# Performance work log

Measured on AMD Instinct MI355X. Metric: run time of the kernel, lower is better.

Reference implementation:

```python
import jax, jax.numpy as jnp
import numpy as np

N_NODES = 100000
N_EDGES = 1600000
DIM = 64
LAYERS = 2


def setup_inputs() -> dict:
    key = jax.random.key(0)
    k1, k2, k3, k4 = jax.random.split(key, 4)
    h = jax.random.normal(k1, (N_NODES, DIM), dtype=jnp.float32)
    w = jax.random.uniform(k2, (N_EDGES,), dtype=jnp.float32)
    src = jax.random.randint(k3, (N_EDGES,), 0, N_NODES, dtype=jnp.int32)
    dst = jax.random.randint(k4, (N_EDGES,), 0, N_NODES, dtype=jnp.int32)
    return {"h": h, "w": w, "src": src, "dst": dst}


def reference(h, w, src, dst):
    N = h.shape[0]
    # weighted in-degree, clamped at 1 (DGL in_degrees(weight='w').clamp(min=1))
    deg = jnp.maximum(jax.ops.segment_sum(w, dst, num_segments=N), 1.0)
    norm = deg[:, None] ** -0.5  # [N, 1]
    embs = [h]
    for _ in range(LAYERS):
        h_norm = h * norm                              # [N, d]
        m = h_norm[src] * w[:, None]                   # [E, d] edge messages (u_mul_e)
        neigh_sum = jax.ops.segment_sum(m, dst, num_segments=N)  # fn.sum
        h = neigh_sum * norm
        embs.append(h)
    # mean over [h0, h1, ..., hL]
    return jnp.mean(jnp.stack(embs, axis=1), axis=1)
```

## Files before the change

kernel.cpp:

```cpp
#include <hip/hip_runtime.h>
#include <hip/hip_bf16.h>

#define D 64
#define THREADS 256
#define BKT_BITS 9
#define BKT_NODES (1 << BKT_BITS)
#define CHUNK 8192

__device__ __forceinline__ unsigned f2bf(float f) {
    unsigned u = __float_as_uint(f);
    return (u + 0x7fffu + ((u >> 16) & 1u)) >> 16;
}
__device__ __forceinline__ float2 bfpair(unsigned v) {
    return make_float2(__uint_as_float(v << 16), __uint_as_float(v & 0xffff0000u));
}

__global__ void p1a_hist(const int* __restrict__ dst, int* __restrict__ blockCount,
                         int E, int B) {
    __shared__ int lc[256];
    int t = threadIdx.x;
    lc[t] = 0;
    __syncthreads();
    int base = blockIdx.x * CHUNK;
    int end = min(base + CHUNK, E);
    for (int e = base + t; e < end; e += THREADS)
        atomicAdd(&lc[dst[e] >> BKT_BITS], 1);
    __syncthreads();
    if (t < B) blockCount[(long long)blockIdx.x * B + t] = lc[t];
}

__global__ void p1b_scanblocks(int* __restrict__ blockCount, int* __restrict__ total,
                               int NBLK, int B) {
    __shared__ int sm[256];
    int b = blockIdx.x, t = threadIdx.x;
    int run = 0;
    for (int base = 0; base < NBLK; base += 256) {
        int i = base + t;
        int v = (i < NBLK) ? blockCount[(long long)i * B + b] : 0;
        sm[t] = v;
        __syncthreads();
        for (int off = 1; off < 256; off <<= 1) {
            int u = (t >= off) ? sm[t - off] : 0;
            __syncthreads();
            sm[t] += u;
            __syncthreads();
        }
        if (i < NBLK) blockCount[(long long)i * B + b] = run + sm[t] - v;
        run += sm[255];
        __syncthreads();
    }
    if (t == 0) total[b] = run;
}

__global__ void p1c_scanbuckets(const int* __restrict__ total, int* __restrict__ bstart,
                                int B, int E) {
    __shared__ int sm[256];
    int t = threadIdx.x;
    int run = 0;
    for (int base = 0; base < B; base += 256) {
        int i = base + t;
        int v = (i < B) ? total[i] : 0;
        sm[t] = v;
        __syncthreads();
        for (int off = 1; off < 256; off <<= 1) {
            int u = (t >= off) ? sm[t - off] : 0;
            __syncthreads();
            sm[t] += u;
            __syncthreads();
        }
        if (i < B) bstart[i] = run + sm[t] - v;
        run += sm[255];
        __syncthreads();
    }
    if (t == 0) bstart[B] = E;
}

__global__ void p1d_scatter(const int* __restrict__ dst, const int* __restrict__ src,
                            const float* __restrict__ w, const int* __restrict__ blockCount,
                            const int* __restrict__ bstart, int2* __restrict__ temp,
                            int E, int B) {
    __shared__ int cur[256];
    int t = threadIdx.x;
    if (t < B) cur[t] = bstart[t] + blockCount[(long long)blockIdx.x * B + t];
    __syncthreads();
    int base = blockIdx.x * CHUNK;
    int end = min(base + CHUNK, E);
    for (int e = base + t; e < end; e += THREADS) {
        int d = dst[e];
        int b = d >> BKT_BITS;
        int pos = atomicAdd(&cur[b], 1);
        temp[pos] = make_int2(src[e] | ((d & (BKT_NODES - 1)) << 17),
                              __float_as_int(w[e]));
    }
}

__global__ void p2_build(const int2* __restrict__ temp, const int* __restrict__ bstart,
                         int2* __restrict__ packed, int* __restrict__ rowptr,
                         float* __restrict__ norm, int N, int E, int B) {
    __shared__ int cnt[BKT_NODES];
    __shared__ float degs[BKT_NODES];
    __shared__ int cur[BKT_NODES];
    __shared__ int sm[256];
    int b = blockIdx.x, t = threadIdx.x;
    int ebeg = bstart[b], eend = bstart[b + 1];
    for (int i = t; i < BKT_NODES; i += THREADS) { cnt[i] = 0; degs[i] = 0.0f; }
    __syncthreads();
    for (int e = ebeg + t; e < eend; e += THREADS) {
        int2 pk = temp[e];
        int dl = (pk.x >> 17) & (BKT_NODES - 1);
        atomicAdd(&cnt[dl], 1);
        atomicAdd(&degs[dl], __int_as_float(pk.y));
    }
    __syncthreads();
    int run = 0;
    for (int base = 0; base < BKT_NODES; base += 256) {
        int v = cnt[base + t];
        sm[t] = v;
        __syncthreads();
        for (int off = 1; off < 256; off <<= 1) {
            int u = (t >= off) ? sm[t - off] : 0;
            __syncthreads();
            sm[t] += u;
            __syncthreads();
        }
        cur[base + t] = run + sm[t] - v;
        run += sm[255];
        __syncthreads();
    }
    int node0 = b << BKT_BITS;
    for (int i = t; i < BKT_NODES; i += THREADS) {
        int node = node0 + i;
        if (node < N) {
            rowptr[node] = ebeg + cur[i];
            norm[node] = rsqrtf(fmaxf(degs[i], 1.0f));
        }
    }
    if (b == 0 && t == 0) rowptr[N] = E;
    __syncthreads();
    for (int e = ebeg + t; e < eend; e += THREADS) {
        int2 pk = temp[e];
        int dl = (pk.x >> 17) & (BKT_NODES - 1);
        int pos = atomicAdd(&cur[dl], 1);
        packed[ebeg + pos] = make_int2(pk.x & 0x1ffff, pk.y);
    }
}

__global__ void tobf16_kernel(const float* __restrict__ h, unsigned* __restrict__ hbf2,
                              long long nd4) {
    long long i = (long long)blockIdx.x * blockDim.x + threadIdx.x;
    if (i < nd4) {
        float4 v = ((const float4*)h)[i];
        ((uint2*)hbf2)[i] = make_uint2(f2bf(v.x) | (f2bf(v.y) << 16),
                                       f2bf(v.z) | (f2bf(v.w) << 16));
    }
}

__global__ void gather1_kernel(const uint2* __restrict__ h_in, const int2* __restrict__ packed,
                               const int* __restrict__ rowptr, const float* __restrict__ norm,
                               uint2* __restrict__ h_out, int N) {
    int node = blockIdx.x * (blockDim.x >> 4) + (threadIdx.x >> 4);
    int lane = threadIdx.x & 15;
    if (node >= N) return;
    int j = rowptr[node], end = rowptr[node + 1];
    float a00 = 0, a01 = 0, a02 = 0, a03 = 0;
    float a10 = 0, a11 = 0, a12 = 0, a13 = 0;
    float a20 = 0, a21 = 0, a22 = 0, a23 = 0;
    float a30 = 0, a31 = 0, a32 = 0, a33 = 0;
    for (; j + 4 <= end; j += 4) {
        int2 p0 = packed[j], p1 = packed[j + 1], p2 = packed[j + 2], p3 = packed[j + 3];
        uint2 r0 = h_in[((long long)p0.x << 4) + lane];
        uint2 r1 = h_in[((long long)p1.x << 4) + lane];
        uint2 r2 = h_in[((long long)p2.x << 4) + lane];
        uint2 r3 = h_in[((long long)p3.x << 4) + lane];
        float c0 = __int_as_float(p0.y) * norm[p0.x];
        float c1 = __int_as_float(p1.y) * norm[p1.x];
        float c2 = __int_as_float(p2.y) * norm[p2.x];
        float c3 = __int_as_float(p3.y) * norm[p3.x];
        float2 f0a = bfpair(r0.x), f0b = bfpair(r0.y);
        float2 f1a = bfpair(r1.x), f1b = bfpair(r1.y);
        float2 f2a = bfpair(r2.x), f2b = bfpair(r2.y);
        float2 f3a = bfpair(r3.x), f3b = bfpair(r3.y);
        a00 = fmaf(f0a.x, c0, a00); a01 = fmaf(f0a.y, c0, a01);
        a02 = fmaf(f0b.x, c0, a02); a03 = fmaf(f0b.y, c0, a03);
        a10 = fmaf(f1a.x, c1, a10); a11 = fmaf(f1a.y, c1, a11);
        a12 = fmaf(f1b.x, c1, a12); a13 = fmaf(f1b.y, c1, a13);
        a20 = fmaf(f2a.x, c2, a20); a21 = fmaf(f2a.y, c2, a21);
        a22 = fmaf(f2b.x, c2, a22); a23 = fmaf(f2b.y, c2, a23);
        a30 = fmaf(f3a.x, c3, a30); a31 = fmaf(f3a.y, c3, a31);
        a32 = fmaf(f3b.x, c3, a32); a33 = fmaf(f3b.y, c3, a33);
    }
    for (; j < end; ++j) {
        int2 p = packed[j];
        uint2 r = h_in[((long long)p.x << 4) + lane];
        float c = __int_as_float(p.y) * norm[p.x];
        float2 fa = bfpair(r.x), fb = bfpair(r.y);
        a00 = fmaf(fa.x, c, a00); a01 = fmaf(fa.y, c, a01);
        a02 = fmaf(fb.x, c, a02); a03 = fmaf(fb.y, c, a03);
    }
    float nv = norm[node];
    float d0 = ((a00 + a10) + (a20 + a30)) * nv;
    float d1 = ((a01 + a11) + (a21 + a31)) * nv;
    float d2 = ((a02 + a12) + (a22 + a32)) * nv;
    float d3 = ((a03 + a13) + (a23 + a33)) * nv;
    h_out[((long long)node << 4) + lane] =
        make_uint2(f2bf(d0) | (f2bf(d1) << 16), f2bf(d2) | (f2bf(d3) << 16));
}

__global__ void gather2_final_kernel(const uint2* __restrict__ h0bf, const uint2* __restrict__ h1bf,
                                     const int2* __restrict__ packed, const int* __restrict__ rowptr,
                                     const float* __restrict__ norm, float* __restrict__ out, int N) {
    int node = blockIdx.x * (blockDim.x >> 4) + (threadIdx.x >> 4);
    int lane = threadIdx.x & 15;
    if (node >= N) return;
    int j = rowptr[node], end = rowptr[node + 1];
    float a00 = 0, a01 = 0, a02 = 0, a03 = 0;
    float a10 = 0, a11 = 0, a12 = 0, a13 = 0;
    float a20 = 0, a21 = 0, a22 = 0, a23 = 0;
    float a30 = 0, a31 = 0, a32 = 0, a33 = 0;
    for (; j + 4 <= end; j += 4) {
        int2 p0 = packed[j], p1 = packed[j + 1], p2 = packed[j + 2], p3 = packed[j + 3];
        uint2 r0 = h1bf[((long long)p0.x << 4) + lane];
        uint2 r1 = h1bf[((long long)p1.x << 4) + lane];
        uint2 r2 = h1bf[((long long)p2.x << 4) + lane];
        uint2 r3 = h1bf[((long long)p3.x << 4) + lane];
        float c0 = __int_as_float(p0.y) * norm[p0.x];
        float c1 = __int_as_float(p1.y) * norm[p1.x];
        float c2 = __int_as_float(p2.y) * norm[p2.x];
        float c3 = __int_as_float(p3.y) * norm[p3.x];
        float2 f0a = bfpair(r0.x), f0b = bfpair(r0.y);
        float2 f1a = bfpair(r1.x), f1b = bfpair(r1.y);
        float2 f2a = bfpair(r2.x), f2b = bfpair(r2.y);
        float2 f3a = bfpair(r3.x), f3b = bfpair(r3.y);
        a00 = fmaf(f0a.x, c0, a00); a01 = fmaf(f0a.y, c0, a01);
        a02 = fmaf(f0b.x, c0, a02); a03 = fmaf(f0b.y, c0, a03);
        a10 = fmaf(f1a.x, c1, a10); a11 = fmaf(f1a.y, c1, a11);
        a12 = fmaf(f1b.x, c1, a12); a13 = fmaf(f1b.y, c1, a13);
        a20 = fmaf(f2a.x, c2, a20); a21 = fmaf(f2a.y, c2, a21);
        a22 = fmaf(f2b.x, c2, a22); a23 = fmaf(f2b.y, c2, a23);
        a30 = fmaf(f3a.x, c3, a30); a31 = fmaf(f3a.y, c3, a31);
        a32 = fmaf(f3b.x, c3, a32); a33 = fmaf(f3b.y, c3, a33);
    }
    for (; j < end; ++j) {
        int2 p = packed[j];
        uint2 r = h1bf[((long long)p.x << 4) + lane];
        float c = __int_as_float(p.y) * norm[p.x];
        float2 fa = bfpair(r.x), fb = bfpair(r.y);
        a00 = fmaf(fa.x, c, a00); a01 = fmaf(fa.y, c, a01);
        a02 = fmaf(fb.x, c, a02); a03 = fmaf(fb.y, c, a03);
    }
    long long idx = ((long long)node << 4) + lane;
    float nv = norm[node];
    uint2 h0r = h0bf[idx], h1r = h1bf[idx];
    float2 h0a = bfpair(h0r.x), h0b = bfpair(h0r.y);
    float2 h1a = bfpair(h1r.x), h1b = bfpair(h1r.y);
    float4 o;
    o.x = (h0a.x + h1a.x + ((a00 + a10) + (a20 + a30)) * nv) * (1.0f / 3.0f);
    o.y = (h0a.y + h1a.y + ((a01 + a11) + (a21 + a31)) * nv) * (1.0f / 3.0f);
    o.z = (h0b.x + h1b.x + ((a02 + a12) + (a22 + a32)) * nv) * (1.0f / 3.0f);
    o.w = (h0b.y + h1b.y + ((a03 + a13) + (a23 + a33)) * nv) * (1.0f / 3.0f);
    ((float4*)out)[idx] = o;
}

extern "C" void kernel_launch(void* const* d_in, const int* in_sizes, int n_in,
                              void* d_out, int out_size, void* d_ws, size_t ws_size,
                              hipStream_t stream) {
    const float* h   = (const float*)d_in[0];
    const float* w   = (const float*)d_in[1];
    const int*   src = (const int*)d_in[2];
    const int*   dst = (const int*)d_in[3];
    const int N = in_sizes[0] / D;
    const int E = in_sizes[1];
    float* out = (float*)d_out;

    const int B = (N + BKT_NODES - 1) >> BKT_BITS;
    const int NBLK = (E + CHUNK - 1) / CHUNK;

    char* ws = (char*)d_ws;
    size_t off = 0;
    auto alloc = [&](size_t bytes, size_t align) -> char* {
        off = (off + align - 1) & ~(align - 1);
        char* p = ws + off;
        off += bytes;
        return p;
    };
    float* norm     = (float*)alloc((size_t)N * 4, 16);
    int*   rowptr   = (int*)  alloc((size_t)(N + 1) * 4, 16);
    int*   total    = (int*)  alloc((size_t)B * 4, 16);
    int*   bstart   = (int*)  alloc((size_t)(B + 1) * 4, 16);
    int*   blockCnt = (int*)  alloc((size_t)NBLK * B * 4, 16);
    int2*  packed   = (int2*) alloc((size_t)E * 8, 16);
    char*  shared_region = alloc((size_t)E * 8, 128);
    int2*     temp = (int2*)shared_region;
    unsigned* h1bf = (unsigned*)shared_region;
    unsigned* h0bf = (unsigned*)alloc((size_t)N * D * 2, 128);

    const int nodes_per_block = THREADS / 16;
    const int gather_blocks = (N + nodes_per_block - 1) / nodes_per_block;
    const long long nd4 = (long long)N * D / 4;
    const int cvt_blocks = (int)((nd4 + THREADS - 1) / THREADS);

    p1a_hist<<<NBLK, THREADS, 0, stream>>>(dst, blockCnt, E, B);
    p1b_scanblocks<<<B, 256, 0, stream>>>(blockCnt, total, NBLK, B);
    p1c_scanbuckets<<<1, 256, 0, stream>>>(total, bstart, B, E);
    p1d_scatter<<<NBLK, THREADS, 0, stream>>>(dst, src, w, blockCnt, bstart, temp, E, B);
    p2_build<<<B, 256, 0, stream>>>(temp, bstart, packed, rowptr, norm, N, E, B);

    tobf16_kernel<<<cvt_blocks, THREADS, 0, stream>>>(h, h0bf, nd4);

    gather1_kernel<<<gather_blocks, THREADS, 0, stream>>>((const uint2*)h0bf, packed, rowptr,
                                                          norm, (uint2*)h1bf, N);
    gather2_final_kernel<<<gather_blocks, THREADS, 0, stream>>>((const uint2*)h0bf, (const uint2*)h1bf,
                                                                packed, rowptr, norm, out, N);
}
```

Before: 234.3 us.

## Pad CSR rows to multiples of four, prefold source norm, use 16B gathers

The CSR build is split into two kernels. The first computes degree norms and padded row starts, with each row rounded up to a multiple of four. The second places edges with the weight already multiplied by norm[src] and fills padding slots with zero-weight entries. The gather kernels then run a tail-free loop that reads edge pairs with int4 loads, drops the per-edge norm gather, and uses 8 lanes per node with 16-byte bf16 row loads instead of 16 lanes with 8-byte loads. The cost is an extra launch, extra padded edge traffic and more registers per thread.

```diff
diff --git a/kernel.cpp b/kernel.cpp
--- a/kernel.cpp
+++ b/kernel.cpp
@@ -6,6 +6,7 @@
 #define BKT_BITS 9
 #define BKT_NODES (1 << BKT_BITS)
 #define CHUNK 8192
+#define PADMAX 1540
 
 __device__ __forceinline__ unsigned f2bf(float f) {
     unsigned u = __float_as_uint(f);
@@ -94,13 +95,13 @@
     }
 }
 
-__global__ void p2_build(const int2* __restrict__ temp, const int* __restrict__ bstart,
-                         int2* __restrict__ packed, int* __restrict__ rowptr,
-                         float* __restrict__ norm, int N, int E, int B) {
+__global__ void p2a_norm(const int2* __restrict__ temp, const int* __restrict__ bstart,
+                         int* __restrict__ rowptrP, float* __restrict__ norm,
+                         int N, int E, int B) {
     __shared__ int cnt[BKT_NODES];
     __shared__ float degs[BKT_NODES];
-    __shared__ int cur[BKT_NODES];
     __shared__ int sm[256];
+    __shared__ int rowst[BKT_NODES];
     int b = blockIdx.x, t = threadIdx.x;
     int ebeg = bstart[b], eend = bstart[b + 1];
     for (int i = t; i < BKT_NODES; i += THREADS) { cnt[i] = 0; degs[i] = 0.0f; }
@@ -114,7 +115,7 @@
     __syncthreads();
     int run = 0;
     for (int base = 0; base < BKT_NODES; base += 256) {
-        int v = cnt[base + t];
+        int v = (cnt[base + t] + 3) & ~3;
         sm[t] = v;
         __syncthreads();
         for (int off = 1; off < 256; off <<= 1) {
@@ -123,25 +124,45 @@
             sm[t] += u;
             __syncthreads();
         }
-        cur[base + t] = run + sm[t] - v;
+        rowst[base + t] = run + sm[t] - v;
         run += sm[255];
         __syncthreads();
     }
+    int pbase = ((ebeg + 3) & ~3) + PADMAX * b;
     int node0 = b << BKT_BITS;
     for (int i = t; i < BKT_NODES; i += THREADS) {
+        rowptrP[node0 + i] = pbase + rowst[i];
         int node = node0 + i;
-        if (node < N) {
-            rowptr[node] = ebeg + cur[i];
-            norm[node] = rsqrtf(fmaxf(degs[i], 1.0f));
-        }
-    }
-    if (b == 0 && t == 0) rowptr[N] = E;
+        if (node < N) norm[node] = rsqrtf(fmaxf(degs[i], 1.0f));
+    }
+    if (b == B - 1 && t == 0)
+        rowptrP[(long long)B << BKT_BITS] = ((E + 3) & ~3) + PADMAX * B;
+}
+
+__global__ void p2b_place(const int2* __restrict__ temp, const int* __restrict__ bstart,
+                          const int* __restrict__ rowptrP, const float* __restrict__ norm,
+                          int2* __restrict__ packed, int N, int B) {
+    __shared__ int cur[BKT_NODES];
+    int b = blockIdx.x, t = threadIdx.x;
+    int ebeg = bstart[b], eend = bstart[b + 1];
+    int node0 = b << BKT_BITS;
+    for (int i = t; i < BKT_NODES; i += THREADS) cur[i] = rowptrP[node0 + i];
     __syncthreads();
     for (int e = ebeg + t; e < eend; e += THREADS) {
         int2 pk = temp[e];
         int dl = (pk.x >> 17) & (BKT_NODES - 1);
+        int s = pk.x & 0x1ffff;
         int pos = atomicAdd(&cur[dl], 1);
-        packed[ebeg + pos] = make_int2(pk.x & 0x1ffff, pk.y);
+        float c = __int_as_float(pk.y) * norm[s];
+        packed[pos] = make_int2(s, __float_as_int(c));
+    }
+    __syncthreads();
+    for (int i = t; i < BKT_NODES; i += THREADS) {
+        int node = node0 + i;
+        if (node >= N) continue;
+        int tail = cur[i];
+        int next = rowptrP[node0 + i + 1];
+        for (int p = tail; p < next; ++p) packed[p] = make_int2(0, 0);
     }
 }
 
@@ -155,110 +176,113 @@
     }
 }
 
-__global__ void gather1_kernel(const uint2* __restrict__ h_in, const int2* __restrict__ packed,
+__global__ void gather1_kernel(const uint4* __restrict__ h_in, const int2* __restrict__ packed,
                                const int* __restrict__ rowptr, const float* __restrict__ norm,
-                               uint2* __restrict__ h_out, int N) {
-    int node = blockIdx.x * (blockDim.x >> 4) + (threadIdx.x >> 4);
-    int lane = threadIdx.x & 15;
+                               uint4* __restrict__ h_out, int N) {
+    int node = blockIdx.x * (blockDim.x >> 3) + (threadIdx.x >> 3);
+    int lane = threadIdx.x & 7;
     if (node >= N) return;
     int j = rowptr[node], end = rowptr[node + 1];
-    float a00 = 0, a01 = 0, a02 = 0, a03 = 0;
-    float a10 = 0, a11 = 0, a12 = 0, a13 = 0;
-    float a20 = 0, a21 = 0, a22 = 0, a23 = 0;
-    float a30 = 0, a31 = 0, a32 = 0, a33 = 0;
-    for (; j + 4 <= end; j += 4) {
-        int2 p0 = packed[j], p1 = packed[j + 1], p2 = packed[j + 2], p3 = packed[j + 3];
-        uint2 r0 = h_in[((long long)p0.x << 4) + lane];
-        uint2 r1 = h_in[((long long)p1.x << 4) + lane];
-        uint2 r2 = h_in[((long long)p2.x << 4) + lane];
-        uint2 r3 = h_in[((long long)p3.x << 4) + lane];
-        float c0 = __int_as_float(p0.y) * norm[p0.x];
-        float c1 = __int_as_float(p1.y) * norm[p1.x];
-        float c2 = __int_as_float(p2.y) * norm[p2.x];
-        float c3 = __int_as_float(p3.y) * norm[p3.x];
-        float2 f0a = bfpair(r0.x), f0b = bfpair(r0.y);
-        float2 f1a = bfpair(r1.x), f1b = bfpair(r1.y);
-        float2 f2a = bfpair(r2.x), f2b = bfpair(r2.y);
-        float2 f3a = bfpair(r3.x), f3b = bfpair(r3.y);
-        a00 = fmaf(f0a.x, c0, a00); a01 = fmaf(f0a.y, c0, a01);
-        a02 = fmaf(f0b.x, c0, a02); a03 = fmaf(f0b.y, c0, a03);
-        a10 = fmaf(f1a.x, c1, a10); a11 = fmaf(f1a.y, c1, a11);
-        a12 = fmaf(f1b.x, c1, a12); a13 = fmaf(f1b.y, c1, a13);
-        a20 = fmaf(f2a.x, c2, a20); a21 = fmaf(f2a.y, c2, a21);
-        a22 = fmaf(f2b.x, c2, a22); a23 = fmaf(f2b.y, c2, a23);
-        a30 = fmaf(f3a.x, c3, a30); a31 = fmaf(f3a.y, c3, a31);
-        a32 = fmaf(f3b.x, c3, a32); a33 = fmaf(f3b.y, c3, a33);
-    }
-    for (; j < end; ++j) {
-        int2 p = packed[j];
-        uint2 r = h_in[((long long)p.x << 4) + lane];
-        float c = __int_as_float(p.y) * norm[p.x];
-        float2 fa = bfpair(r.x), fb = bfpair(r.y);
-        a00 = fmaf(fa.x, c, a00); a01 = fmaf(fa.y, c, a01);
-        a02 = fmaf(fb.x, c, a02); a03 = fmaf(fb.y, c, a03);
+    float acc[4][8];
+#pragma unroll
+    for (int u = 0; u < 4; ++u)
+#pragma unroll
+        for (int k = 0; k < 8; ++k) acc[u][k] = 0.0f;
+    for (; j < end; j += 4) {
+        int4 q0 = *(const int4*)(packed + j);
+        int4 q1 = *(const int4*)(packed + j + 2);
+        uint4 r0 = h_in[((long long)q0.x << 3) + lane];
+        uint4 r1 = h_in[((long long)q0.z << 3) + lane];
+        uint4 r2 = h_in[((long long)q1.x << 3) + lane];
+        uint4 r3 = h_in[((long long)q1.z << 3) + lane];
+        float c0 = __int_as_float(q0.y), c1 = __int_as_float(q0.w);
+        float c2 = __int_as_float(q1.y), c3 = __int_as_float(q1.w);
+        float2 f;
+        f = bfpair(r0.x); acc[0][0] = fmaf(f.x, c0, acc[0][0]); acc[0][1] = fmaf(f.y, c0, acc[0][1]);
+        f = bfpair(r0.y); acc[0][2] = fmaf(f.x, c0, acc[0][2]); acc[0][3] = fmaf(f.y, c0, acc[0][3]);
+        f = bfpair(r0.z); acc[0][4] = fmaf(f.x, c0, acc[0][4]); acc[0][5] = fmaf(f.y, c0, acc[0][5]);
+        f = bfpair(r0.w); acc[0][6] = fmaf(f.x, c0, acc[0][6]); acc[0][7] = fmaf(f.y, c0, acc[0][7]);
+        f = bfpair(r1.x); acc[1][0] = fmaf(f.x, c1, acc[1][0]); acc[1][1] = fmaf(f.y, c1, acc[1][1]);
+        f = bfpair(r1.y); acc[1][2] = fmaf(f.x, c1, acc[1][2]); acc[1][3] = fmaf(f.y, c1, acc[1][3]);
+        f = bfpair(r1.z); acc[1][4] = fmaf(f.x, c1, acc[1][4]); acc[1][5] = fmaf(f.y, c1, acc[1][5]);
+        f = bfpair(r1.w); acc[1][6] = fmaf(f.x, c1, acc[1][6]); acc[1][7] = fmaf(f.y, c1, acc[1][7]);
+        f = bfpair(r2.x); acc[2][0] = fmaf(f.x, c2, acc[2][0]); acc[2][1] = fmaf(f.y, c2, acc[2][1]);
+        f = bfpair(r2.y); acc[2][2] = fmaf(f.x, c2, acc[2][2]); acc[2][3] = fmaf(f.y, c2, acc[2][3]);
+        f = bfpair(r2.z); acc[2][4] = fmaf(f.x, c2, acc[2][4]); acc[2][5] = fmaf(f.y, c2, acc[2][5]);
+        f = bfpair(r2.w); acc[2][6] = fmaf(f.x, c2, acc[2][6]); acc[2][7] = fmaf(f.y, c2, acc[2][7]);
+        f = bfpair(r3.x); acc[3][0] = fmaf(f.x, c3, acc[3][0]); acc[3][1] = fmaf(f.y, c3, acc[3][1]);
+        f = bfpair(r3.y); acc[3][2] = fmaf(f.x, c3, acc[3][2]); acc[3][3] = fmaf(f.y, c3, acc[3][3]);
+        f = bfpair(r3.z); acc[3][4] = fmaf(f.x, c3, acc[3][4]); acc[3][5] = fmaf(f.y, c3, acc[3][5]);
+        f = bfpair(r3.w); acc[3][6] = fmaf(f.x, c3, acc[3][6]); acc[3][7] = fmaf(f.y, c3, acc[3][7]);
     }
     float nv = norm[node];
-    float d0 = ((a00 + a10) + (a20 + a30)) * nv;
-    float d1 = ((a01 + a11) + (a21 + a31)) * nv;
-    float d2 = ((a02 + a12) + (a22 + a32)) * nv;
-    float d3 = ((a03 + a13) + (a23 + a33)) * nv;
-    h_out[((long long)node << 4) + lane] =
-        make_uint2(f2bf(d0) | (f2bf(d1) << 16), f2bf(d2) | (f2bf(d3) << 16));
-}
-
-__global__ void gather2_final_kernel(const uint2* __restrict__ h0bf, const uint2* __restrict__ h1bf,
+    float d[8];
+#pragma unroll
+    for (int k = 0; k < 8; ++k)
+        d[k] = ((acc[0][k] + acc[1][k]) + (acc[2][k] + acc[3][k])) * nv;
+    uint4 o;
+    o.x = f2bf(d[0]) | (f2bf(d[1]) << 16);
+    o.y = f2bf(d[2]) | (f2bf(d[3]) << 16);
+    o.z = f2bf(d[4]) | (f2bf(d[5]) << 16);
+    o.w = f2bf(d[6]) | (f2bf(d[7]) << 16);
+    h_out[((long long)node << 3) + lane] = o;
+}
+
+__global__ void gather2_final_kernel(const uint4* __restrict__ h0bf, const uint4* __restrict__ h1bf,
                                      const int2* __restrict__ packed, const int* __restrict__ rowptr,
                                      const float* __restrict__ norm, float* __restrict__ out, int N) {
-    int node = blockIdx.x * (blockDim.x >> 4) + (threadIdx.x >> 4);
-    int lane = threadIdx.x & 15;
+    int node = blockIdx.x * (blockDim.x >> 3) + (threadIdx.x >> 3);
+    int lane = threadIdx.x & 7;
     if (node >= N) return;
     int j = rowptr[node], end = rowptr[node + 1];
-    float a00 = 0, a01 = 0, a02 = 0, a03 = 0;
-    float a10 = 0, a11 = 0, a12 = 0, a13 = 0;
-    float a20 = 0, a21 = 0, a22 = 0, a23 = 0;
-    float a30 = 0, a31 = 0, a32 = 0, a33 = 0;
-    for (; j + 4 <= end; j += 4) {
-        int2 p0 = packed[j], p1 = packed[j + 1], p2 = packed[j + 2], p3 = packed[j + 3];
-        uint2 r0 = h1bf[((long long)p0.x << 4) + lane];
-        uint2 r1 = h1bf[((long long)p1.x << 4) + lane];
-        uint2 r2 = h1bf[((long long)p2.x << 4) + lane];
-        uint2 r3 = h1bf[((long long)p3.x << 4) + lane];
-        float c0 = __int_as_float(p0.y) * norm[p0.x];
-        float c1 = __int_as_float(p1.y) * norm[p1.x];
-        float c2 = __int_as_float(p2.y) * norm[p2.x];
-        float c3 = __int_as_float(p3.y) * norm[p3.x];
-        float2 f0a = bfpair(r0.x), f0b = bfpair(r0.y);
-        float2 f1a = bfpair(r1.x), f1b = bfpair(r1.y);
-        float2 f2a = bfpair(r2.x), f2b = bfpair(r2.y);
-        float2 f3a = bfpair(r3.x), f3b = bfpair(r3.y);
-        a00 = fmaf(f0a.x, c0, a00); a01 = fmaf(f0a.y, c0, a01);
-        a02 = fmaf(f0b.x, c0, a02); a03 = fmaf(f0b.y, c0, a03);
-        a10 = fmaf(f1a.x, c1, a10); a11 = fmaf(f1a.y, c1, a11);
-        a12 = fmaf(f1b.x, c1, a12); a13 = fmaf(f1b.y, c1, a13);
-        a20 = fmaf(f2a.x, c2, a20); a21 = fmaf(f2a.y, c2, a21);
-        a22 = fmaf(f2b.x, c2, a22); a23 = fmaf(f2b.y, c2, a23);
-        a30 = fmaf(f3a.x, c3, a30); a31 = fmaf(f3a.y, c3, a31);
-        a32 = fmaf(f3b.x, c3, a32); a33 = fmaf(f3b.y, c3, a33);
-    }
-    for (; j < end; ++j) {
-        int2 p = packed[j];
-        uint2 r = h1bf[((long long)p.x << 4) + lane];
-        float c = __int_as_float(p.y) * norm[p.x];
-        float2 fa = bfpair(r.x), fb = bfpair(r.y);
-        a00 = fmaf(fa.x, c, a00); a01 = fmaf(fa.y, c, a01);
-        a02 = fmaf(fb.x, c, a02); a03 = fmaf(fb.y, c, a03);
-    }
-    long long idx = ((long long)node << 4) + lane;
+    float acc[4][8];
+#pragma unroll
+    for (int u = 0; u < 4; ++u)
+#pragma unroll
+        for (int k = 0; k < 8; ++k) acc[u][k] = 0.0f;
+    for (; j < end; j += 4) {
+        int4 q0 = *(const int4*)(packed + j);
+        int4 q1 = *(const int4*)(packed + j + 2);
+        uint4 r0 = h1bf[((long long)q0.x << 3) + lane];
+        uint4 r1 = h1bf[((long long)q0.z << 3) + lane];
+        uint4 r2 = h1bf[((long long)q1.x << 3) + lane];
+        uint4 r3 = h1bf[((long long)q1.z << 3) + lane];
+        float c0 = __int_as_float(q0.y), c1 = __int_as_float(q0.w);
+        float c2 = __int_as_float(q1.y), c3 = __int_as_float(q1.w);
+        float2 f;
+        f = bfpair(r0.x); acc[0][0] = fmaf(f.x, c0, acc[0][0]); acc[0][1] = fmaf(f.y, c0, acc[0][1]);
+        f = bfpair(r0.y); acc[0][2] = fmaf(f.x, c0, acc[0][2]); acc[0][3] = fmaf(f.y, c0, acc[0][3]);
+        f = bfpair(r0.z); acc[0][4] = fmaf(f.x, c0, acc[0][4]); acc[0][5] = fmaf(f.y, c0, acc[0][5]);
+        f = bfpair(r0.w); acc[0][6] = fmaf(f.x, c0, acc[0][6]); acc[0][7] = fmaf(f.y, c0, acc[0][7]);
+        f = bfpair(r1.x); acc[1][0] = fmaf(f.x, c1, acc[1][0]); acc[1][1] = fmaf(f.y, c1, acc[1][1]);
+        f = bfpair(r1.y); acc[1][2] = fmaf(f.x, c1, acc[1][2]); acc[1][3] = fmaf(f.y, c1, acc[1][3]);
+        f = bfpair(r1.z); acc[1][4] = fmaf(f.x, c1, acc[1][4]); acc[1][5] = fmaf(f.y, c1, acc[1][5]);
+        f = bfpair(r1.w); acc[1][6] = fmaf(f.x, c1, acc[1][6]); acc[1][7] = fmaf(f.y, c1, acc[1][7]);
+        f = bfpair(r2.x); acc[2][0] = fmaf(f.x, c2, acc[2][0]); acc[2][1] = fmaf(f.y, c2, acc[2][1]);
+        f = bfpair(r2.y); acc[2][2] = fmaf(f.x, c2, acc[2][2]); acc[2][3] = fmaf(f.y, c2, acc[2][3]);
+        f = bfpair(r2.z); acc[2][4] = fmaf(f.x, c2, acc[2][4]); acc[2][5] = fmaf(f.y, c2, acc[2][5]);
+        f = bfpair(r2.w); acc[2][6] = fmaf(f.x, c2, acc[2][6]); acc[2][7] = fmaf(f.y, c2, acc[2][7]);
+        f = bfpair(r3.x); acc[3][0] = fmaf(f.x, c3, acc[3][0]); acc[3][1] = fmaf(f.y, c3, acc[3][1]);
+        f = bfpair(r3.y); acc[3][2] = fmaf(f.x, c3, acc[3][2]); acc[3][3] = fmaf(f.y, c3, acc[3][3]);
+        f = bfpair(r3.z); acc[3][4] = fmaf(f.x, c3, acc[3][4]); acc[3][5] = fmaf(f.y, c3, acc[3][5]);
+        f = bfpair(r3.w); acc[3][6] = fmaf(f.x, c3, acc[3][6]); acc[3][7] = fmaf(f.y, c3, acc[3][7]);
+    }
+    long long idx = ((long long)node << 3) + lane;
     float nv = norm[node];
-    uint2 h0r = h0bf[idx], h1r = h1bf[idx];
-    float2 h0a = bfpair(h0r.x), h0b = bfpair(h0r.y);
-    float2 h1a = bfpair(h1r.x), h1b = bfpair(h1r.y);
-    float4 o;
-    o.x = (h0a.x + h1a.x + ((a00 + a10) + (a20 + a30)) * nv) * (1.0f / 3.0f);
-    o.y = (h0a.y + h1a.y + ((a01 + a11) + (a21 + a31)) * nv) * (1.0f / 3.0f);
-    o.z = (h0b.x + h1b.x + ((a02 + a12) + (a22 + a32)) * nv) * (1.0f / 3.0f);
-    o.w = (h0b.y + h1b.y + ((a03 + a13) + (a23 + a33)) * nv) * (1.0f / 3.0f);
-    ((float4*)out)[idx] = o;
+    uint4 h0r = h0bf[idx], h1r = h1bf[idx];
+    float2 h0p[4] = { bfpair(h0r.x), bfpair(h0r.y), bfpair(h0r.z), bfpair(h0r.w) };
+    float2 h1p[4] = { bfpair(h1r.x), bfpair(h1r.y), bfpair(h1r.z), bfpair(h1r.w) };
+    float4 o0, o1;
+    o0.x = (h0p[0].x + h1p[0].x + ((acc[0][0] + acc[1][0]) + (acc[2][0] + acc[3][0])) * nv) * (1.0f / 3.0f);
+    o0.y = (h0p[0].y + h1p[0].y + ((acc[0][1] + acc[1][1]) + (acc[2][1] + acc[3][1])) * nv) * (1.0f / 3.0f);
+    o0.z = (h0p[1].x + h1p[1].x + ((acc[0][2] + acc[1][2]) + (acc[2][2] + acc[3][2])) * nv) * (1.0f / 3.0f);
+    o0.w = (h0p[1].y + h1p[1].y + ((acc[0][3] + acc[1][3]) + (acc[2][3] + acc[3][3])) * nv) * (1.0f / 3.0f);
+    o1.x = (h0p[2].x + h1p[2].x + ((acc[0][4] + acc[1][4]) + (acc[2][4] + acc[3][4])) * nv) * (1.0f / 3.0f);
+    o1.y = (h0p[2].y + h1p[2].y + ((acc[0][5] + acc[1][5]) + (acc[2][5] + acc[3][5])) * nv) * (1.0f / 3.0f);
+    o1.z = (h0p[3].x + h1p[3].x + ((acc[0][6] + acc[1][6]) + (acc[2][6] + acc[3][6])) * nv) * (1.0f / 3.0f);
+    o1.w = (h0p[3].y + h1p[3].y + ((acc[0][7] + acc[1][7]) + (acc[2][7] + acc[3][7])) * nv) * (1.0f / 3.0f);
+    ((float4*)out)[((long long)node << 4) + (lane << 1)] = o0;
+    ((float4*)out)[((long long)node << 4) + (lane << 1) + 1] = o1;
 }
 
 extern "C" void kernel_launch(void* const* d_in, const int* in_sizes, int n_in,
@@ -274,6 +298,7 @@
 
     const int B = (N + BKT_NODES - 1) >> BKT_BITS;
     const int NBLK = (E + CHUNK - 1) / CHUNK;
+    const int EPAD = ((E + 3) & ~3) + PADMAX * B;
 
     char* ws = (char*)d_ws;
     size_t off = 0;
@@ -284,17 +309,17 @@
         return p;
     };
     float* norm     = (float*)alloc((size_t)N * 4, 16);
-    int*   rowptr   = (int*)  alloc((size_t)(N + 1) * 4, 16);
+    int*   rowptrP  = (int*)  alloc(((size_t)B * BKT_NODES + 1) * 4, 16);
     int*   total    = (int*)  alloc((size_t)B * 4, 16);
     int*   bstart   = (int*)  alloc((size_t)(B + 1) * 4, 16);
     int*   blockCnt = (int*)  alloc((size_t)NBLK * B * 4, 16);
-    int2*  packed   = (int2*) alloc((size_t)E * 8, 16);
+    int2*  packed   = (int2*) alloc((size_t)EPAD * 8, 16);
     char*  shared_region = alloc((size_t)E * 8, 128);
     int2*     temp = (int2*)shared_region;
     unsigned* h1bf = (unsigned*)shared_region;
     unsigned* h0bf = (unsigned*)alloc((size_t)N * D * 2, 128);
 
-    const int nodes_per_block = THREADS / 16;
+    const int nodes_per_block = THREADS / 8;
     const int gather_blocks = (N + nodes_per_block - 1) / nodes_per_block;
     const long long nd4 = (long long)N * D / 4;
     const int cvt_blocks = (int)((nd4 + THREADS - 1) / THREADS);
@@ -303,12 +328,13 @@
     p1b_scanblocks<<<B, 256, 0, stream>>>(blockCnt, total, NBLK, B);
     p1c_scanbuckets<<<1, 256, 0, stream>>>(total, bstart, B, E);
     p1d_scatter<<<NBLK, THREADS, 0, stream>>>(dst, src, w, blockCnt, bstart, temp, E, B);
-    p2_build<<<B, 256, 0, stream>>>(temp, bstart, packed, rowptr, norm, N, E, B);
+    p2a_norm<<<B, 256, 0, stream>>>(temp, bstart, rowptrP, norm, N, E, B);
+    p2b_place<<<B, 256, 0, stream>>>(temp, bstart, rowptrP, norm, packed, N, B);
 
     tobf16_kernel<<<cvt_blocks, THREADS, 0, stream>>>(h, h0bf, nd4);
 
-    gather1_kernel<<<gather_blocks, THREADS, 0, stream>>>((const uint2*)h0bf, packed, rowptr,
-                                                          norm, (uint2*)h1bf, N);
-    gather2_final_kernel<<<gather_blocks, THREADS, 0, stream>>>((const uint2*)h0bf, (const uint2*)h1bf,
-                                                                packed, rowptr, norm, out, N);
-}
+    gather1_kernel<<<gather_blocks, THREADS, 0, stream>>>((const uint4*)h0bf, packed, rowptrP,
+                                                          norm, (uint4*)h1bf, N);
+    gather2_final_kernel<<<gather_blocks, THREADS, 0, stream>>>((const uint4*)h0bf, (const uint4*)h1bf,
+                                                                packed, rowptrP, norm, out, N);
+}
```

New measurement: 538.0 us. +129.6%, slower.
